# Optimization experiments

Hardware: AMD Instinct MI355X
Metric: run time of the kernel (lower is better)

Reference implementation:

```python
import jax, jax.numpy as jnp
import numpy as np

LN_EPS = 1e-5

def _layernorm(x, gamma, beta):
    mu = jnp.mean(x, axis=-1, keepdims=True)
    var = jnp.mean(jnp.square(x - mu), axis=-1, keepdims=True)
    return (x - mu) * jax.lax.rsqrt(var + LN_EPS) * gamma + beta

def _gcn_layer(A_hat, H, W, b, g, beta):
    # batched dense-equivalent of per-batch torch.sparse.mm: (B,N,N)@(B,N,F)
    H = jnp.einsum('bnm,bmf->bnf', A_hat, H)
    H = H @ W + b            # Linear
    H = _layernorm(H, g, beta)
    return jax.nn.relu(H)    # dropout is identity in eval

def setup_inputs() -> dict:
    key = jax.random.key(0)
    ks = jax.random.split(key, 8)
    B, N, F, Hd, K, G = 16, 2048, 64, 256, 128, 18
    fuse = Hd + G  # 274
    return {
        'A_hat': jax.random.uniform(ks[0], (B, N, N), dtype=jnp.float32),
        'X': jax.random.normal(ks[1], (B, N, F), dtype=jnp.float32),
        'global_vec': jax.random.normal(ks[2], (B, G), dtype=jnp.float32),
        'W1': jax.random.normal(ks[3], (F, Hd), dtype=jnp.float32) / np.sqrt(F),
        'b1': jnp.zeros((Hd,), jnp.float32),
        'g1': jnp.ones((Hd,), jnp.float32),
        'beta1': jnp.zeros((Hd,), jnp.float32),
        'W2': jax.random.normal(ks[4], (Hd, Hd), dtype=jnp.float32) / np.sqrt(Hd),
        'b2': jnp.zeros((Hd,), jnp.float32),
        'g2': jnp.ones((Hd,), jnp.float32),
        'beta2': jnp.zeros((Hd,), jnp.float32),
        'Ws': jax.random.normal(ks[5], (fuse, 1), dtype=jnp.float32) / np.sqrt(fuse),
        'bs': jnp.zeros((1,), jnp.float32),
        'Wa': jax.random.normal(ks[6], (fuse, K), dtype=jnp.float32) / np.sqrt(fuse),
        'ba': jnp.zeros((K,), jnp.float32),
    }

def reference(A_hat, X, global_vec, W1, b1, g1, beta1, W2, b2, g2, beta2, Ws, bs, Wa, ba):
    H = _gcn_layer(A_hat, X, W1, b1, g1, beta1)
    H = _gcn_layer(A_hat, H, W2, b2, g2, beta2)
    gcnout = jnp.mean(H, axis=1)                       # 'mean' readout -> (B, hidden)
    fused = jnp.concatenate([gcnout, global_vec], axis=-1)  # (B, hidden+18)
    pred_y_reg = (fused @ Ws + bs)[:, 0]               # (B,)
    pred_arr_reg = fused @ Wa + ba                     # (B, K)
    return pred_y_reg, pred_arr_reg
```

## Files before the change

### kernel.cpp

```cpp
#include <hip/hip_runtime.h>

typedef unsigned short u16;
typedef __attribute__((ext_vector_type(8))) short bf16x8;
typedef __attribute__((ext_vector_type(4))) float f32x4;

__device__ __forceinline__ unsigned f2bf(float f) {
  unsigned u = __float_as_uint(f);
  return (u + 0x7fffu + ((u >> 16) & 1u)) >> 16;
}

__device__ __forceinline__ void async16(const u16* g, u16* l) {
  __builtin_amdgcn_global_load_lds(
      (const __attribute__((address_space(1))) void*)g,
      (__attribute__((address_space(3))) void*)l, 16, 0, 0);
}

template<int BN, bool AF32, bool CBF16>
__global__ __launch_bounds__(256, 2) void gemm_tile(
    const void* __restrict__ Av, const u16* __restrict__ Bt, void* __restrict__ Cv,
    int K, int lda, int ldb, int ldc,
    long long sA, long long sB, long long sC)
{
  constexpr int BM = 128, BK = 32, PAD = BK + 8;
  __shared__ __align__(16) u16 As[BM * PAD];
  __shared__ __align__(16) u16 Bs[BN * PAD];
  const int tid  = threadIdx.x;
  const int w    = tid >> 6;
  const int lane = tid & 63;
  const int l15  = lane & 15, quad = lane >> 4;
  const int m0 = blockIdx.x * BM, n0 = blockIdx.y * BN;
  const int bz = blockIdx.z;

  const u16* Bp = Bt + (size_t)sB * bz;

  f32x4 acc[2][BN / 16];
#pragma unroll
  for (int i = 0; i < 2; i++)
#pragma unroll
    for (int j = 0; j < BN / 16; j++)
#pragma unroll
      for (int r = 0; r < 4; r++) acc[i][j][r] = 0.f;

  for (int k0 = 0; k0 < K; k0 += BK) {
    __syncthreads();
    if constexpr (AF32) {
      const float* Af = (const float*)Av + (size_t)sA * bz;
      const int r = tid >> 3, c = (tid & 7) << 2;
#pragma unroll
      for (int rr = 0; rr < 4; rr++) {
        const int row = rr * 32 + r;
        const float4 v = *(const float4*)(Af + (size_t)(m0 + row) * lda + k0 + c);
        uint2 p;
        p.x = f2bf(v.x) | (f2bf(v.y) << 16);
        p.y = f2bf(v.z) | (f2bf(v.w) << 16);
        *(uint2*)(As + row * PAD + c) = p;
      }
    } else {
      const u16* Ah = (const u16*)Av + (size_t)sA * bz;
      const int r = tid >> 2, c = (tid & 3) << 3;
#pragma unroll
      for (int rr = 0; rr < 2; rr++) {
        const int row = rr * 64 + r;
        *(uint4*)(As + row * PAD + c) =
            *(const uint4*)(Ah + (size_t)(m0 + row) * lda + k0 + c);
      }
    }
    {
      const int r = tid >> 2, c = (tid & 3) << 3;
#pragma unroll
      for (int p = 0; p < BN / 64; p++) {
        const int n = p * 64 + r;
        *(uint4*)(Bs + n * PAD + c) =
            *(const uint4*)(Bp + (size_t)(n0 + n) * ldb + k0 + c);
      }
    }
    __syncthreads();
    const bf16x8 a0 = *(const bf16x8*)(As + (w * 32 + l15) * PAD + quad * 8);
    const bf16x8 a1 = *(const bf16x8*)(As + (w * 32 + 16 + l15) * PAD + quad * 8);
#pragma unroll
    for (int nt = 0; nt < BN / 16; nt++) {
      const bf16x8 bv = *(const bf16x8*)(Bs + (nt * 16 + l15) * PAD + quad * 8);
      acc[0][nt] = __builtin_amdgcn_mfma_f32_16x16x32_bf16(a0, bv, acc[0][nt], 0, 0, 0);
      acc[1][nt] = __builtin_amdgcn_mfma_f32_16x16x32_bf16(a1, bv, acc[1][nt], 0, 0, 0);
    }
  }
#pragma unroll
  for (int mt = 0; mt < 2; mt++)
#pragma unroll
    for (int nt = 0; nt < BN / 16; nt++)
#pragma unroll
      for (int rg = 0; rg < 4; rg++) {
        const size_t row = (size_t)m0 + w * 32 + mt * 16 + quad * 4 + rg;
        const size_t col = (size_t)n0 + nt * 16 + l15;
        if constexpr (CBF16)
          *((u16*)Cv + (size_t)sC * bz + row * ldc + col) = (u16)f2bf(acc[mt][nt][rg]);
        else
          *((float*)Cv + (size_t)sC * bz + row * ldc + col) = acc[mt][nt][rg];
      }
}

template<bool AF32, bool MEAN>
__global__ __launch_bounds__(256, 2) void gcn_gemm(
    const void* __restrict__ Av, const u16* __restrict__ Bt,
    const float* __restrict__ bias, const float* __restrict__ gam,
    const float* __restrict__ bet, u16* __restrict__ H, float* __restrict__ gcn)
{
  constexpr int BK = 64;
  __shared__ __align__(16) u16 As[64 * BK];
  __shared__ __align__(16) u16 Bs[256 * BK];
  __shared__ float colsum[256];
  const int tid = threadIdx.x;
  const int w = tid >> 6, lane = tid & 63, l15 = lane & 15, quad = lane >> 4;
  const int m0 = blockIdx.x * 64;
  const int bz = blockIdx.y;

  f32x4 acc[16];
#pragma unroll
  for (int nt = 0; nt < 16; nt++)
#pragma unroll
    for (int r = 0; r < 4; r++) acc[nt][r] = 0.f;

  const int sr = tid >> 3, sc = (tid & 7) << 3;
  const u16* Bg = Bt + (size_t)bz * 524288 + (size_t)sr * 2048 + sc;
  u16* lA = As + tid * 8;
  u16* lB = Bs + tid * 8;
  const float* Af = nullptr;
  const u16* Ag = nullptr;
  if constexpr (AF32)
    Af = (const float*)Av + (size_t)bz * 4194304 + (size_t)(m0 + sr) * 2048 + sc;
  else
    Ag = (const u16*)Av + (size_t)bz * 4194304 + (size_t)(m0 + sr) * 2048 + sc;

  for (int k0 = 0; k0 < 2048; k0 += BK) {
    __syncthreads();
    if constexpr (AF32) {
#pragma unroll
      for (int q = 0; q < 2; q++) {
        const float* p = Af + (size_t)q * 32 * 2048 + k0;
        const float4 v0 = *(const float4*)p;
        const float4 v1 = *(const float4*)(p + 4);
        uint4 r;
        r.x = f2bf(v0.x) | (f2bf(v0.y) << 16);
        r.y = f2bf(v0.z) | (f2bf(v0.w) << 16);
        r.z = f2bf(v1.x) | (f2bf(v1.y) << 16);
        r.w = f2bf(v1.z) | (f2bf(v1.w) << 16);
        *(uint4*)(lA + q * 2048) = r;
      }
    } else {
#pragma unroll
      for (int q = 0; q < 2; q++)
        async16(Ag + (size_t)q * 32 * 2048 + k0, lA + q * 2048);
    }
#pragma unroll
    for (int p = 0; p < 8; p++)
      async16(Bg + (size_t)p * 65536 + k0, lB + p * 2048);
    __syncthreads();
#pragma unroll
    for (int kk = 0; kk < 2; kk++) {
      const bf16x8 a = *(const bf16x8*)(As + (w * 16 + l15) * BK + kk * 32 + quad * 8);
#pragma unroll
      for (int nt = 0; nt < 16; nt++) {
        const bf16x8 b = *(const bf16x8*)(Bs + (nt * 16 + l15) * BK + kk * 32 + quad * 8);
        acc[nt] = __builtin_amdgcn_mfma_f32_16x16x32_bf16(a, b, acc[nt], 0, 0, 0);
      }
    }
  }

  float s[4] = {0.f, 0.f, 0.f, 0.f};
#pragma unroll
  for (int nt = 0; nt < 16; nt++) {
    const float bv = bias[nt * 16 + l15];
#pragma unroll
    for (int rg = 0; rg < 4; rg++) { acc[nt][rg] += bv; s[rg] += acc[nt][rg]; }
  }
#pragma unroll
  for (int off = 8; off >= 1; off >>= 1)
#pragma unroll
    for (int rg = 0; rg < 4; rg++) s[rg] += __shfl_xor(s[rg], off);
  float mu[4], qv[4] = {0.f, 0.f, 0.f, 0.f};
#pragma unroll
  for (int rg = 0; rg < 4; rg++) mu[rg] = s[rg] * (1.f / 256.f);
#pragma unroll
  for (int nt = 0; nt < 16; nt++)
#pragma unroll
    for (int rg = 0; rg < 4; rg++) {
      const float d = acc[nt][rg] - mu[rg];
      qv[rg] += d * d;
    }
#pragma unroll
  for (int off = 8; off >= 1; off >>= 1)
#pragma unroll
    for (int rg = 0; rg < 4; rg++) qv[rg] += __shfl_xor(qv[rg], off);
  float inv[4];
#pragma unroll
  for (int rg = 0; rg < 4; rg++) inv[rg] = rsqrtf(qv[rg] * (1.f / 256.f) + 1e-5f);

  if constexpr (!MEAN) {
#pragma unroll
    for (int nt = 0; nt < 16; nt++) {
      const float gv = gam[nt * 16 + l15], ev = bet[nt * 16 + l15];
#pragma unroll
      for (int rg = 0; rg < 4; rg++) {
        const float y = fmaxf((acc[nt][rg] - mu[rg]) * inv[rg] * gv + ev, 0.f);
        const size_t row = (size_t)bz * 2048 + m0 + w * 16 + quad * 4 + rg;
        H[row * 256 + nt * 16 + l15] = (u16)f2bf(y);
      }
    }
  } else {
    colsum[tid] = 0.f;
    __syncthreads();
#pragma unroll
    for (int nt = 0; nt < 16; nt++) {
      const float gv = gam[nt * 16 + l15], ev = bet[nt * 16 + l15];
      float p = 0.f;
#pragma unroll
      for (int rg = 0; rg < 4; rg++)
        p += fmaxf((acc[nt][rg] - mu[rg]) * inv[rg] * gv + ev, 0.f);
      p += __shfl_xor(p, 16);
      p += __shfl_xor(p, 32);
      if (quad == 0) atomicAdd(&colsum[nt * 16 + l15], p);
    }
    __syncthreads();
    atomicAdd(gcn + bz * 256 + tid, colsum[tid]);
  }
}

__global__ __launch_bounds__(256) void convert_bf16(const float* __restrict__ in,
                                                    u16* __restrict__ out, long long n8)
{
  const long long i = (long long)blockIdx.x * 256 + threadIdx.x;
  if (i >= n8) return;
  const float4 a = ((const float4*)in)[2 * i];
  const float4 b = ((const float4*)in)[2 * i + 1];
  uint4 r;
  r.x = f2bf(a.x) | (f2bf(a.y) << 16);
  r.y = f2bf(a.z) | (f2bf(a.w) << 16);
  r.z = f2bf(b.x) | (f2bf(b.y) << 16);
  r.w = f2bf(b.z) | (f2bf(b.w) << 16);
  ((uint4*)out)[i] = r;
}

__global__ __launch_bounds__(256) void transpose_bf16(const float* __restrict__ in,
                                                      u16* __restrict__ outp,
                                                      int rows, int cols)
{
  const int n = rows * cols;
  const int o = blockIdx.x * 256 + threadIdx.x;
  if (o < n) {
    const int c = o / rows, r = o - c * rows;
    outp[o] = (u16)f2bf(in[r * cols + c]);
  }
}

__global__ void zero_kernel(float* p, int n) {
  const int i = blockIdx.x * 256 + threadIdx.x;
  if (i < n) p[i] = 0.f;
}

__global__ __launch_bounds__(128) void final_kernel(
    const float* __restrict__ gcn, const float* __restrict__ gv,
    const float* __restrict__ Ws, const float* __restrict__ bs,
    const float* __restrict__ Wa, const float* __restrict__ ba,
    float* __restrict__ out)
{
  const int b = blockIdx.x, t = threadIdx.x;
  __shared__ float fused[274];
  fused[t] = gcn[b * 256 + t] * (1.f / 2048.f);
  fused[128 + t] = gcn[b * 256 + 128 + t] * (1.f / 2048.f);
  if (t < 18) fused[256 + t] = gv[b * 18 + t];
  __syncthreads();
  float acc = ba[t];
  for (int i = 0; i < 274; i++) acc = fmaf(fused[i], Wa[i * 128 + t], acc);
  out[16 + b * 128 + t] = acc;
  if (t < 64) {
    float p = 0.f;
    for (int i = t; i < 274; i += 64) p += fused[i] * Ws[i];
#pragma unroll
    for (int off = 32; off >= 1; off >>= 1) p += __shfl_xor(p, off);
    if (t == 0) out[b] = p + bs[0];
  }
}

extern "C" void kernel_launch(void* const* d_in, const int* in_sizes, int n_in,
                              void* d_out, int out_size, void* d_ws, size_t ws_size,
                              hipStream_t stream)
{
  const float* A   = (const float*)d_in[0];
  const float* X   = (const float*)d_in[1];
  const float* GV  = (const float*)d_in[2];
  const float* W1  = (const float*)d_in[3];
  const float* b1  = (const float*)d_in[4];
  const float* g1  = (const float*)d_in[5];
  const float* be1 = (const float*)d_in[6];
  const float* W2  = (const float*)d_in[7];
  const float* b2  = (const float*)d_in[8];
  const float* g2  = (const float*)d_in[9];
  const float* be2 = (const float*)d_in[10];
  const float* Ws  = (const float*)d_in[11];
  const float* bs  = (const float*)d_in[12];
  const float* Wa  = (const float*)d_in[13];
  const float* ba  = (const float*)d_in[14];
  float* out = (float*)d_out;
  (void)in_sizes; (void)n_in; (void)out_size;

  const bool big = ws_size >= (size_t)188923904;
  char* ws   = (char*)d_ws;
  u16*  Abf  = (u16*)ws;
  char* base = big ? ws + 134217728 : ws;
  u16*   Xbf = (u16*)(base + 0);
  u16*   W1T = (u16*)(base + 4194304);
  u16*   W2T = (u16*)(base + 4227072);
  u16*   XWT = (u16*)(base + 4358144);
  u16*   H1  = (u16*)(base + 21135360);
  u16*   HWT = (u16*)(base + 37912576);
  float* GCN = (float*)(base + 54689792);

  zero_kernel<<<16, 256, 0, stream>>>(GCN, 4096);
  convert_bf16<<<1024, 256, 0, stream>>>(X, Xbf, 262144LL);
  transpose_bf16<<<64, 256, 0, stream>>>(W1, W1T, 64, 256);
  transpose_bf16<<<256, 256, 0, stream>>>(W2, W2T, 256, 256);
  if (big) convert_bf16<<<32768, 256, 0, stream>>>(A, Abf, 8388608LL);

  gemm_tile<128, false, true><<<dim3(2, 16, 16), 256, 0, stream>>>(
      W1T, Xbf, XWT, 64, 64, 64, 2048, 0LL, 131072LL, 524288LL);

  if (big)
    gcn_gemm<false, false><<<dim3(32, 16), 256, 0, stream>>>(
        Abf, XWT, b1, g1, be1, H1, nullptr);
  else
    gcn_gemm<true, false><<<dim3(32, 16), 256, 0, stream>>>(
        A, XWT, b1, g1, be1, H1, nullptr);

  gemm_tile<128, false, true><<<dim3(2, 16, 16), 256, 0, stream>>>(
      W2T, H1, HWT, 256, 256, 256, 2048, 0LL, 524288LL, 524288LL);

  if (big)
    gcn_gemm<false, true><<<dim3(32, 16), 256, 0, stream>>>(
        Abf, HWT, b2, g2, be2, nullptr, GCN);
  else
    gcn_gemm<true, true><<<dim3(32, 16), 256, 0, stream>>>(
        A, HWT, b2, g2, be2, nullptr, GCN);

  final_kernel<<<16, 128, 0, stream>>>(GCN, GV, Ws, bs, Wa, ba, out);
}
```

Before: 654.4 us.

## Rework GCN aggregation GEMM to 32x32 MFMA with register-resident A tiles

The gcn_gemm kernel now loads fp32 A_hat directly into registers, converts it to bf16 and feeds it straight to MFMA, with no LDS staging for A. It switches from 16x16x32 to 32x32x16 MFMA, with each wave covering 64 rows by 64 columns and the B tile stored in LDS under an XOR swizzle. The separate A_hat bf16 pre-conversion pass and the 'big' workspace branch are removed, so both layers read fp32 A directly. Because each wave now holds only part of a row, the LayerNorm statistics need a cross-wave reduction through LDS with extra barriers, and A global loads are no longer coalesced across a row tile.

```diff
diff --git a/kernel.cpp b/kernel.cpp
--- a/kernel.cpp
+++ b/kernel.cpp
@@ -3,6 +3,7 @@
 typedef unsigned short u16;
 typedef __attribute__((ext_vector_type(8))) short bf16x8;
 typedef __attribute__((ext_vector_type(4))) float f32x4;
+typedef __attribute__((ext_vector_type(16))) float f32x16;
 
 __device__ __forceinline__ unsigned f2bf(float f) {
   unsigned u = __float_as_uint(f);
@@ -99,129 +100,176 @@
       }
 }
 
-template<bool AF32, bool MEAN>
+template<bool MEAN>
 __global__ __launch_bounds__(256, 2) void gcn_gemm(
-    const void* __restrict__ Av, const u16* __restrict__ Bt,
+    const float* __restrict__ A, const u16* __restrict__ Bt,
     const float* __restrict__ bias, const float* __restrict__ gam,
     const float* __restrict__ bet, u16* __restrict__ H, float* __restrict__ gcn)
 {
-  constexpr int BK = 64;
-  __shared__ __align__(16) u16 As[64 * BK];
-  __shared__ __align__(16) u16 Bs[256 * BK];
-  __shared__ float colsum[256];
+  __shared__ __align__(16) u16 Bs[256 * 64];
   const int tid = threadIdx.x;
-  const int w = tid >> 6, lane = tid & 63, l15 = lane & 15, quad = lane >> 4;
+  const int w = tid >> 6, lane = tid & 63;
+  const int l31 = lane & 31, half = lane >> 5;
   const int m0 = blockIdx.x * 64;
   const int bz = blockIdx.y;
 
-  f32x4 acc[16];
-#pragma unroll
-  for (int nt = 0; nt < 16; nt++)
-#pragma unroll
-    for (int r = 0; r < 4; r++) acc[nt][r] = 0.f;
-
-  const int sr = tid >> 3, sc = (tid & 7) << 3;
-  const u16* Bg = Bt + (size_t)bz * 524288 + (size_t)sr * 2048 + sc;
-  u16* lA = As + tid * 8;
+  f32x16 acc[2][2];
+#pragma unroll
+  for (int i = 0; i < 2; i++)
+#pragma unroll
+    for (int j = 0; j < 2; j++)
+#pragma unroll
+      for (int r = 0; r < 16; r++) acc[i][j][r] = 0.f;
+
+  const int tn = tid >> 3;
+  const int clog = (tid & 7) ^ (tn & 7);
+  const u16* Bg = Bt + (size_t)bz * 524288 + (size_t)tn * 2048 + clog * 8;
   u16* lB = Bs + tid * 8;
-  const float* Af = nullptr;
-  const u16* Ag = nullptr;
-  if constexpr (AF32)
-    Af = (const float*)Av + (size_t)bz * 4194304 + (size_t)(m0 + sr) * 2048 + sc;
-  else
-    Ag = (const u16*)Av + (size_t)bz * 4194304 + (size_t)(m0 + sr) * 2048 + sc;
-
-  for (int k0 = 0; k0 < 2048; k0 += BK) {
+
+  const float* Ag = A + (size_t)bz * 4194304 + (size_t)(m0 + l31) * 2048 + half * 8;
+
+  for (int k0 = 0; k0 < 2048; k0 += 64) {
     __syncthreads();
-    if constexpr (AF32) {
-#pragma unroll
-      for (int q = 0; q < 2; q++) {
-        const float* p = Af + (size_t)q * 32 * 2048 + k0;
+#pragma unroll
+    for (int p = 0; p < 8; p++)
+      async16(Bg + (size_t)p * 65536 + k0, lB + p * 2048);
+    bf16x8 a[2][4];
+#pragma unroll
+    for (int mt = 0; mt < 2; mt++)
+#pragma unroll
+      for (int kk = 0; kk < 4; kk++) {
+        const float* p = Ag + (size_t)mt * 65536 + k0 + kk * 16;
         const float4 v0 = *(const float4*)p;
         const float4 v1 = *(const float4*)(p + 4);
-        uint4 r;
-        r.x = f2bf(v0.x) | (f2bf(v0.y) << 16);
-        r.y = f2bf(v0.z) | (f2bf(v0.w) << 16);
-        r.z = f2bf(v1.x) | (f2bf(v1.y) << 16);
-        r.w = f2bf(v1.z) | (f2bf(v1.w) << 16);
-        *(uint4*)(lA + q * 2048) = r;
-      }
-    } else {
-#pragma unroll
-      for (int q = 0; q < 2; q++)
-        async16(Ag + (size_t)q * 32 * 2048 + k0, lA + q * 2048);
-    }
-#pragma unroll
-    for (int p = 0; p < 8; p++)
-      async16(Bg + (size_t)p * 65536 + k0, lB + p * 2048);
+        union { bf16x8 v; uint4 u; } r;
+        r.u.x = f2bf(v0.x) | (f2bf(v0.y) << 16);
+        r.u.y = f2bf(v0.z) | (f2bf(v0.w) << 16);
+        r.u.z = f2bf(v1.x) | (f2bf(v1.y) << 16);
+        r.u.w = f2bf(v1.z) | (f2bf(v1.w) << 16);
+        a[mt][kk] = r.v;
+      }
     __syncthreads();
 #pragma unroll
-    for (int kk = 0; kk < 2; kk++) {
-      const bf16x8 a = *(const bf16x8*)(As + (w * 16 + l15) * BK + kk * 32 + quad * 8);
-#pragma unroll
-      for (int nt = 0; nt < 16; nt++) {
-        const bf16x8 b = *(const bf16x8*)(Bs + (nt * 16 + l15) * BK + kk * 32 + quad * 8);
-        acc[nt] = __builtin_amdgcn_mfma_f32_16x16x32_bf16(a, b, acc[nt], 0, 0, 0);
-      }
-    }
-  }
-
-  float s[4] = {0.f, 0.f, 0.f, 0.f};
-#pragma unroll
-  for (int nt = 0; nt < 16; nt++) {
-    const float bv = bias[nt * 16 + l15];
-#pragma unroll
-    for (int rg = 0; rg < 4; rg++) { acc[nt][rg] += bv; s[rg] += acc[nt][rg]; }
-  }
-#pragma unroll
-  for (int off = 8; off >= 1; off >>= 1)
-#pragma unroll
-    for (int rg = 0; rg < 4; rg++) s[rg] += __shfl_xor(s[rg], off);
-  float mu[4], qv[4] = {0.f, 0.f, 0.f, 0.f};
-#pragma unroll
-  for (int rg = 0; rg < 4; rg++) mu[rg] = s[rg] * (1.f / 256.f);
-#pragma unroll
-  for (int nt = 0; nt < 16; nt++)
-#pragma unroll
-    for (int rg = 0; rg < 4; rg++) {
-      const float d = acc[nt][rg] - mu[rg];
-      qv[rg] += d * d;
-    }
-#pragma unroll
-  for (int off = 8; off >= 1; off >>= 1)
-#pragma unroll
-    for (int rg = 0; rg < 4; rg++) qv[rg] += __shfl_xor(qv[rg], off);
-  float inv[4];
-#pragma unroll
-  for (int rg = 0; rg < 4; rg++) inv[rg] = rsqrtf(qv[rg] * (1.f / 256.f) + 1e-5f);
-
+    for (int kk = 0; kk < 4; kk++)
+#pragma unroll
+      for (int nt = 0; nt < 2; nt++) {
+        const int n = w * 64 + nt * 32 + l31;
+        const int pc = (kk * 2 + half) ^ (l31 & 7);
+        const bf16x8 b = *(const bf16x8*)(Bs + n * 64 + pc * 8);
+        acc[0][nt] = __builtin_amdgcn_mfma_f32_32x32x16_bf16(a[0][kk], b, acc[0][nt], 0, 0, 0);
+        acc[1][nt] = __builtin_amdgcn_mfma_f32_32x32x16_bf16(a[1][kk], b, acc[1][nt], 0, 0, 0);
+      }
+  }
+
+  const int col0 = w * 64 + l31;
+  const float b0 = bias[col0], b1 = bias[col0 + 32];
+  float s2[2][16];
+#pragma unroll
+  for (int mt = 0; mt < 2; mt++)
+#pragma unroll
+    for (int r = 0; r < 16; r++) {
+      acc[mt][0][r] += b0;
+      acc[mt][1][r] += b1;
+      s2[mt][r] = acc[mt][0][r] + acc[mt][1][r];
+    }
+#pragma unroll
+  for (int off = 1; off <= 16; off <<= 1)
+#pragma unroll
+    for (int mt = 0; mt < 2; mt++)
+#pragma unroll
+      for (int r = 0; r < 16; r++) s2[mt][r] += __shfl_xor(s2[mt][r], off);
+
+  float* sm = (float*)Bs;
+  __syncthreads();
+  if (l31 == 0) {
+#pragma unroll
+    for (int mt = 0; mt < 2; mt++)
+#pragma unroll
+      for (int r = 0; r < 16; r++) {
+        const int rl = (r & 3) + 8 * (r >> 2) + 4 * half;
+        sm[w * 64 + mt * 32 + rl] = s2[mt][r];
+      }
+  }
+  __syncthreads();
+  if (tid < 64)
+    sm[256 + tid] = (sm[tid] + sm[64 + tid] + sm[128 + tid] + sm[192 + tid]) * (1.f / 256.f);
+  __syncthreads();
+  float4 mu4[2][4];
+#pragma unroll
+  for (int mt = 0; mt < 2; mt++)
+#pragma unroll
+    for (int g = 0; g < 4; g++)
+      mu4[mt][g] = *(const float4*)(sm + 256 + mt * 32 + g * 8 + 4 * half);
+
+  float q2[2][16];
+#pragma unroll
+  for (int mt = 0; mt < 2; mt++)
+#pragma unroll
+    for (int r = 0; r < 16; r++) {
+      const float mu = ((const float*)&mu4[mt][r >> 2])[r & 3];
+      const float d0 = acc[mt][0][r] - mu, d1 = acc[mt][1][r] - mu;
+      q2[mt][r] = d0 * d0 + d1 * d1;
+    }
+#pragma unroll
+  for (int off = 1; off <= 16; off <<= 1)
+#pragma unroll
+    for (int mt = 0; mt < 2; mt++)
+#pragma unroll
+      for (int r = 0; r < 16; r++) q2[mt][r] += __shfl_xor(q2[mt][r], off);
+  if (l31 == 0) {
+#pragma unroll
+    for (int mt = 0; mt < 2; mt++)
+#pragma unroll
+      for (int r = 0; r < 16; r++) {
+        const int rl = (r & 3) + 8 * (r >> 2) + 4 * half;
+        sm[w * 64 + mt * 32 + rl] = q2[mt][r];
+      }
+  }
+  __syncthreads();
+  if (tid < 64)
+    sm[320 + tid] = rsqrtf(
+        (sm[tid] + sm[64 + tid] + sm[128 + tid] + sm[192 + tid]) * (1.f / 256.f) + 1e-5f);
+  __syncthreads();
+  float4 iv4[2][4];
+#pragma unroll
+  for (int mt = 0; mt < 2; mt++)
+#pragma unroll
+    for (int g = 0; g < 4; g++)
+      iv4[mt][g] = *(const float4*)(sm + 320 + mt * 32 + g * 8 + 4 * half);
+
+  const float g0 = gam[col0], g1 = gam[col0 + 32];
+  const float e0 = bet[col0], e1 = bet[col0 + 32];
   if constexpr (!MEAN) {
 #pragma unroll
-    for (int nt = 0; nt < 16; nt++) {
-      const float gv = gam[nt * 16 + l15], ev = bet[nt * 16 + l15];
-#pragma unroll
-      for (int rg = 0; rg < 4; rg++) {
-        const float y = fmaxf((acc[nt][rg] - mu[rg]) * inv[rg] * gv + ev, 0.f);
-        const size_t row = (size_t)bz * 2048 + m0 + w * 16 + quad * 4 + rg;
-        H[row * 256 + nt * 16 + l15] = (u16)f2bf(y);
-      }
-    }
+    for (int mt = 0; mt < 2; mt++)
+#pragma unroll
+      for (int r = 0; r < 16; r++) {
+        const float mu = ((const float*)&mu4[mt][r >> 2])[r & 3];
+        const float iv = ((const float*)&iv4[mt][r >> 2])[r & 3];
+        const int rl = (r & 3) + 8 * (r >> 2) + 4 * half;
+        const size_t row = (size_t)bz * 2048 + m0 + mt * 32 + rl;
+        const float y0 = fmaxf((acc[mt][0][r] - mu) * iv * g0 + e0, 0.f);
+        const float y1 = fmaxf((acc[mt][1][r] - mu) * iv * g1 + e1, 0.f);
+        H[row * 256 + col0]      = (u16)f2bf(y0);
+        H[row * 256 + col0 + 32] = (u16)f2bf(y1);
+      }
   } else {
-    colsum[tid] = 0.f;
-    __syncthreads();
-#pragma unroll
-    for (int nt = 0; nt < 16; nt++) {
-      const float gv = gam[nt * 16 + l15], ev = bet[nt * 16 + l15];
-      float p = 0.f;
-#pragma unroll
-      for (int rg = 0; rg < 4; rg++)
-        p += fmaxf((acc[nt][rg] - mu[rg]) * inv[rg] * gv + ev, 0.f);
-      p += __shfl_xor(p, 16);
-      p += __shfl_xor(p, 32);
-      if (quad == 0) atomicAdd(&colsum[nt * 16 + l15], p);
-    }
-    __syncthreads();
-    atomicAdd(gcn + bz * 256 + tid, colsum[tid]);
+    float c0 = 0.f, c1 = 0.f;
+#pragma unroll
+    for (int mt = 0; mt < 2; mt++)
+#pragma unroll
+      for (int r = 0; r < 16; r++) {
+        const float mu = ((const float*)&mu4[mt][r >> 2])[r & 3];
+        const float iv = ((const float*)&iv4[mt][r >> 2])[r & 3];
+        c0 += fmaxf((acc[mt][0][r] - mu) * iv * g0 + e0, 0.f);
+        c1 += fmaxf((acc[mt][1][r] - mu) * iv * g1 + e1, 0.f);
+      }
+    c0 += __shfl_xor(c0, 32);
+    c1 += __shfl_xor(c1, 32);
+    if (half == 0) {
+      atomicAdd(gcn + bz * 256 + col0, c0);
+      atomicAdd(gcn + bz * 256 + col0 + 32, c1);
+    }
   }
 }
 
@@ -301,12 +349,9 @@
   const float* Wa  = (const float*)d_in[13];
   const float* ba  = (const float*)d_in[14];
   float* out = (float*)d_out;
-  (void)in_sizes; (void)n_in; (void)out_size;
-
-  const bool big = ws_size >= (size_t)188923904;
-  char* ws   = (char*)d_ws;
-  u16*  Abf  = (u16*)ws;
-  char* base = big ? ws + 134217728 : ws;
+  (void)in_sizes; (void)n_in; (void)out_size; (void)ws_size;
+
+  char* base = (char*)d_ws;
   u16*   Xbf = (u16*)(base + 0);
   u16*   W1T = (u16*)(base + 4194304);
   u16*   W2T = (u16*)(base + 4227072);
@@ -319,27 +364,16 @@
   convert_bf16<<<1024, 256, 0, stream>>>(X, Xbf, 262144LL);
   transpose_bf16<<<64, 256, 0, stream>>>(W1, W1T, 64, 256);
   transpose_bf16<<<256, 256, 0, stream>>>(W2, W2T, 256, 256);
-  if (big) convert_bf16<<<32768, 256, 0, stream>>>(A, Abf, 8388608LL);
 
   gemm_tile<128, false, true><<<dim3(2, 16, 16), 256, 0, stream>>>(
       W1T, Xbf, XWT, 64, 64, 64, 2048, 0LL, 131072LL, 524288LL);
 
-  if (big)
-    gcn_gemm<false, false><<<dim3(32, 16), 256, 0, stream>>>(
-        Abf, XWT, b1, g1, be1, H1, nullptr);
-  else
-    gcn_gemm<true, false><<<dim3(32, 16), 256, 0, stream>>>(
-        A, XWT, b1, g1, be1, H1, nullptr);
+  gcn_gemm<false><<<dim3(32, 16), 256, 0, stream>>>(A, XWT, b1, g1, be1, H1, nullptr);
 
   gemm_tile<128, false, true><<<dim3(2, 16, 16), 256, 0, stream>>>(
       W2T, H1, HWT, 256, 256, 256, 2048, 0LL, 524288LL, 524288LL);
 
-  if (big)
-    gcn_gemm<false, true><<<dim3(32, 16), 256, 0, stream>>>(
-        Abf, HWT, b2, g2, be2, nullptr, GCN);
-  else
-    gcn_gemm<true, true><<<dim3(32, 16), 256, 0, stream>>>(
-        A, HWT, b2, g2, be2, nullptr, GCN);
+  gcn_gemm<true><<<dim3(32, 16), 256, 0, stream>>>(A, HWT, b2, g2, be2, nullptr, GCN);
 
   final_kernel<<<16, 128, 0, stream>>>(GCN, GV, Ws, bs, Wa, ba, out);
 }
```

Result: slower. 730.6 us (+11.6%).
